# Optimization experiments

Measured on AMD Instinct MI355X. Metric: run time of the kernel, lower is better.

The kernel has to match this reference:

```python
import jax, jax.numpy as jnp
import numpy as np

E, K, MULT = 8, 2, 4          # num_experts, top_k, ffn mult
CF = 1.25                     # capacity_factor


def setup_inputs() -> dict:
    key = jax.random.key(0)
    ks = jax.random.split(key, 8)
    B, T, C = 4, 2048, 1024
    H = C * MULT
    s = 0.02
    return {
        "x": jax.random.normal(ks[0], (B, T, C), jnp.float32),
        "rw": jax.random.normal(ks[1], (E, C), jnp.float32) * s,   # router weight [E,C]
        "rb": jnp.zeros((E,), jnp.float32),                        # router bias
        "w1": jax.random.normal(ks[2], (E, C, H), jnp.float32) * s,
        "b1": jnp.zeros((E, H), jnp.float32),
        "w2": jax.random.normal(ks[3], (E, H, C), jnp.float32) * s,
        "b2": jnp.zeros((E, C), jnp.float32),
    }


def reference(x, rw, rb, w1, b1, w2, b2):
    B, T, C = x.shape
    N = B * T
    cap = int(CF * N / E)                      # static capacity per expert
    xf = x.reshape(N, C)
    logits = xf @ rw.T + rb                    # [N,E]
    probs = jax.nn.softmax(logits, axis=-1)
    topk_probs, topk_idx = jax.lax.top_k(probs, K)      # [N,K]
    topk_probs = topk_probs / topk_probs.sum(-1, keepdims=True)

    # Flatten (token, choice) row-major == torch.where(mask) ordering
    flat_idx = topk_idx.reshape(-1)            # [N*K] expert id per slot
    flat_gate = topk_probs.reshape(-1)         # [N*K]
    onehot = jax.nn.one_hot(flat_idx, E, dtype=jnp.int32)          # [N*K,E]
    pos = (jnp.cumsum(onehot, axis=0) - 1)[jnp.arange(N * K), flat_idx]  # rank within expert
    keep = pos < cap                           # first-come-first-served capacity drop
    tok = jnp.arange(N * K) // K               # owning token of each slot

    # Dispatch into [E, cap] buffers; dropped slots go to a dump slot at the end
    buf = jnp.where(keep, flat_idx * cap + pos, E * cap)
    gate_buf = jnp.zeros(E * cap + 1, x.dtype).at[buf].add(flat_gate)[:E * cap]
    tok_buf = jnp.zeros(E * cap + 1, jnp.int32).at[buf].set(tok)[:E * cap]

    inp = xf[tok_buf].reshape(E, cap, C)       # gathered expert inputs
    h = jax.nn.gelu(jnp.einsum('eic,ech->eih', inp, w1) + b1[:, None, :], approximate=False)
    out = jnp.einsum('eih,ehc->eic', h, w2) + b2[:, None, :]
    out = out * gate_buf.reshape(E, cap, 1)    # empty slots have gate 0 -> zero contribution

    y = jnp.zeros((N, C), x.dtype).at[tok_buf].add(out.reshape(E * cap, C))

    # Aux load-balancing loss
    imp = probs.sum(0)
    imp = imp / imp.sum()
    load = jnp.minimum(onehot.sum(0).astype(x.dtype), cap)   # kept token counts
    load = load / load.sum()
    aux_loss = (imp * load).sum() * (E ** 2)
    return y.reshape(B, T, C), aux_loss
```

## Files before the change

kernel.cpp:

```cpp
#include <hip/hip_runtime.h>
#include <hip/hip_bf16.h>
#include <math.h>

#define NE    8
#define KTOP  2
#define CDIM  1024
#define HDIM  4096
#define NTOK  8192
#define CAPE  1280
#define NSLOT (NTOK * KTOP)

typedef __bf16 bf16x8 __attribute__((ext_vector_type(8)));
typedef __bf16 bf16x4 __attribute__((ext_vector_type(4)));
typedef __bf16 bf16x2 __attribute__((ext_vector_type(2)));
typedef float  f32x4  __attribute__((ext_vector_type(4)));

#define GAS __attribute__((address_space(1)))
#define LAS __attribute__((address_space(3)))

__global__ __launch_bounds__(256) void k_transpose_bf16(
    const float* __restrict__ src, __bf16* __restrict__ dst, int R, int Cc)
{
    __shared__ float tile[32][33];
    const int e  = blockIdx.z;
    const int cb = blockIdx.x * 32;
    const int rb = blockIdx.y * 32;
    const int t  = threadIdx.x;
    const int tx = t & 31, ty = t >> 5;
    const float* s = src + (size_t)e * R * Cc;
    __bf16*      d = dst + (size_t)e * R * Cc;
#pragma unroll
    for (int i = 0; i < 32; i += 8)
        tile[ty + i][tx] = s[(size_t)(rb + ty + i) * Cc + cb + tx];
    __syncthreads();
    const int op  = t & 15;
    const int oc0 = t >> 4;
#pragma unroll
    for (int j = 0; j < 2; ++j) {
        const int oc = oc0 + j * 16;
        bf16x2 v;
        v[0] = (__bf16)tile[op * 2][oc];
        v[1] = (__bf16)tile[op * 2 + 1][oc];
        *(bf16x2*)(d + (size_t)(cb + oc) * R + rb + op * 2) = v;
    }
}

__global__ __launch_bounds__(256) void k_router(
    const float* __restrict__ x, const float* __restrict__ rw,
    const float* __restrict__ rb, float* __restrict__ probs,
    float* __restrict__ gates, int* __restrict__ tidx)
{
    __shared__ float rws[NE * CDIM];
    const int tid = threadIdx.x;
    for (int i = tid; i < NE * CDIM / 4; i += 256)
        ((float4*)rws)[i] = ((const float4*)rw)[i];
    __syncthreads();

    const int wave = tid >> 6, lane = tid & 63;
    const int n = blockIdx.x * 4 + wave;
    const float* xr = x + (size_t)n * CDIM;

    float acc[NE];
#pragma unroll
    for (int e = 0; e < NE; ++e) acc[e] = 0.f;
    for (int j = 0; j < CDIM / 64; ++j) {
        const float xv = xr[j * 64 + lane];
#pragma unroll
        for (int e = 0; e < NE; ++e) acc[e] += xv * rws[e * CDIM + j * 64 + lane];
    }
#pragma unroll
    for (int off = 32; off > 0; off >>= 1) {
#pragma unroll
        for (int e = 0; e < NE; ++e) acc[e] += __shfl_down(acc[e], off);
    }
    if (lane == 0) {
        float mx = -1e30f;
#pragma unroll
        for (int e = 0; e < NE; ++e) { acc[e] += rb[e]; mx = fmaxf(mx, acc[e]); }
        float p[NE], s = 0.f;
#pragma unroll
        for (int e = 0; e < NE; ++e) { p[e] = expf(acc[e] - mx); s += p[e]; }
        const float inv = 1.f / s;
#pragma unroll
        for (int e = 0; e < NE; ++e) { p[e] *= inv; probs[(size_t)n * NE + e] = p[e]; }
        int   i1 = 0;  float v1 = p[0];
        int   i2 = -1; float v2 = -1.f;
#pragma unroll
        for (int e = 1; e < NE; ++e) {
            if (p[e] > v1)      { v2 = v1; i2 = i1; v1 = p[e]; i1 = e; }
            else if (p[e] > v2) { v2 = p[e]; i2 = e; }
        }
        const float gs = 1.f / (v1 + v2);
        gates[n * 2 + 0] = v1 * gs;  gates[n * 2 + 1] = v2 * gs;
        tidx[n * 2 + 0]  = i1;       tidx[n * 2 + 1]  = i2;
    }
}

__global__ __launch_bounds__(256) void k_scan(
    const int* __restrict__ tidx, const float* __restrict__ probs,
    int* __restrict__ slot, int* __restrict__ tok, float* __restrict__ d_aux)
{
    __shared__ int   lcnt[256][NE];
    __shared__ float ps[256][NE];
    const int t = threadIdx.x;

    for (int i = t; i < NE * CAPE; i += 256) tok[i] = 0;

    int c8[NE];
#pragma unroll
    for (int e = 0; e < NE; ++e) c8[e] = 0;
    const int per  = NSLOT / 256;
    const int base = t * per;
    for (int s = 0; s < per; ++s) c8[tidx[base + s]]++;
#pragma unroll
    for (int e = 0; e < NE; ++e) lcnt[t][e] = c8[e];

    float f8[NE];
#pragma unroll
    for (int e = 0; e < NE; ++e) f8[e] = 0.f;
    for (int n = t; n < NTOK; n += 256) {
        const float4 a = *(const float4*)(probs + (size_t)n * NE);
        const float4 b = *(const float4*)(probs + (size_t)n * NE + 4);
        f8[0] += a.x; f8[1] += a.y; f8[2] += a.z; f8[3] += a.w;
        f8[4] += b.x; f8[5] += b.y; f8[6] += b.z; f8[7] += b.w;
    }
#pragma unroll
    for (int e = 0; e < NE; ++e) ps[t][e] = f8[e];

    __syncthreads();

    int pre[NE], tot[NE];
#pragma unroll
    for (int e = 0; e < NE; ++e) { pre[e] = 0; tot[e] = 0; }
    for (int tt = 0; tt < 256; ++tt) {
#pragma unroll
        for (int e = 0; e < NE; ++e) {
            const int v = lcnt[tt][e];
            tot[e] += v;
            if (tt < t) pre[e] += v;
        }
    }
    for (int s = 0; s < per; ++s) {
        const int sg = base + s;
        const int e  = tidx[sg];
        const int p  = pre[e]++;
        if (p < CAPE) { slot[sg] = e * CAPE + p; tok[e * CAPE + p] = sg >> 1; }
        else          { slot[sg] = -1; }
    }
    if (t == 0) {
        float imp[NE], isum = 0.f, ld[NE], lsum = 0.f;
#pragma unroll
        for (int e = 0; e < NE; ++e) {
            float v = 0.f;
            for (int tt = 0; tt < 256; ++tt) v += ps[tt][e];
            imp[e] = v; isum += v;
        }
#pragma unroll
        for (int e = 0; e < NE; ++e) { ld[e] = fminf((float)tot[e], (float)CAPE); lsum += ld[e]; }
        float aux = 0.f;
#pragma unroll
        for (int e = 0; e < NE; ++e) aux += (imp[e] / isum) * (ld[e] / lsum);
        *d_aux = aux * (float)(NE * NE);
    }
}

__global__ __launch_bounds__(256) void k_gather(
    const float* __restrict__ x, const int* __restrict__ tok,
    __bf16* __restrict__ inp)
{
    const int row = blockIdx.x;
    const int t   = threadIdx.x;
    const int tk  = tok[row];
    const float4 v = ((const float4*)(x + (size_t)tk * CDIM))[t];
    bf16x4 o;
    o[0] = (__bf16)v.x; o[1] = (__bf16)v.y; o[2] = (__bf16)v.z; o[3] = (__bf16)v.w;
    *(bf16x4*)(inp + (size_t)row * CDIM + t * 4) = o;
}

#define MFMA_BF16 __builtin_amdgcn_mfma_f32_16x16x32_bf16
#define DSR(dst, addr, IMM) \
    asm volatile("ds_read_b128 %0, %1 offset:" #IMM : "=v"(dst) : "v"(addr))
#define WLG(N)  asm volatile("s_waitcnt lgkmcnt(" #N ")" ::: "memory")
#define WVM0()  asm volatile("s_waitcnt vmcnt(0)" ::: "memory")
#define SB0()   __builtin_amdgcn_sched_barrier(0)

#define MFMA_PHASE(MB, AR)                                                    \
    __builtin_amdgcn_s_setprio(1);                                            \
    _Pragma("unroll")                                                         \
    for (int mm = 0; mm < 2; ++mm) {                                          \
        _Pragma("unroll")                                                     \
        for (int n = 0; n < 4; ++n) {                                         \
            acc[(MB) + mm][n] = MFMA_BF16(bfr[n][0], AR[mm][0], acc[(MB) + mm][n], 0, 0, 0); \
            acc[(MB) + mm][n] = MFMA_BF16(bfr[n][1], AR[mm][1], acc[(MB) + mm][n], 0, 0, 0); \
        }                                                                     \
    }                                                                         \
    __builtin_amdgcn_s_setprio(0);                                            \
    SB0();

template <bool GELU>
__global__ __launch_bounds__(512, 2) void k_gemm8(
    const __bf16* __restrict__ Aall, const __bf16* __restrict__ Ball,
    const float* __restrict__ biasAll, __bf16* __restrict__ Call,
    int Ktot, int Ntot, int NBN, int mtPerE)
{
    __shared__ char lds[131072];

    const int NK  = Ktot >> 6;
    const int cpx = gridDim.x >> 3;
    const int id  = blockIdx.x;
    const int sid = (id & 7) * cpx + (id >> 3);
    const int bm  = sid / NBN, bn = sid % NBN;
    const int e   = bm / mtPerE;

    const size_t row0 = (size_t)bm * 256;
    const int    col0 = bn * 256;

    const int tid = threadIdx.x;
    const int w   = tid >> 6, l = tid & 63;
    const int wr  = w >> 2, wc = w & 3;
    const int lr  = l & 15, hi = l >> 4;

    const int srow = (w << 3) + (l >> 3);
    const int kf   = ((l & 7) ^ (l >> 3)) << 3;
    const __bf16* pA = Aall + (row0 + srow) * (size_t)Ktot + kf;
    const __bf16* pB = Ball + ((size_t)e * Ntot + col0 + srow) * (size_t)Ktot + kf;
    const size_t rstep = (size_t)64 * Ktot;
    const unsigned L0  = (unsigned)(size_t)(LAS char*)lds;
    const unsigned dA0 = L0 + w * 1024;
    const unsigned dB0 = L0 + 32768 + w * 1024;

    auto STAGE_ALL = [&](unsigned bufbit, int kt) {
        const __bf16* ga = pA + (size_t)kt * 64;
        const __bf16* gb = pB + (size_t)kt * 64;
#pragma unroll
        for (int h = 0; h < 4; ++h)
            __builtin_amdgcn_global_load_lds(
                (const GAS void*)(ga + h * rstep),
                (LAS void*)(size_t)(dA0 + bufbit + h * 8192), 16, 0, 0);
#pragma unroll
        for (int h = 0; h < 4; ++h)
            __builtin_amdgcn_global_load_lds(
                (const GAS void*)(gb + h * rstep),
                (LAS void*)(size_t)(dB0 + bufbit + h * 8192), 16, 0, 0);
    };

    const unsigned swz = (l & 7) << 4;
    const unsigned kb0 = ((unsigned)(hi << 4)) ^ swz;
    const unsigned kb1 = ((unsigned)(64 + (hi << 4))) ^ swz;
    const unsigned Abase = L0 + wr * 16384 + lr * 128;
    const unsigned Bbase = L0 + 32768 + (wc >> 1) * 16384 + (wc & 1) * 8192 + lr * 128;

    STAGE_ALL(0, 0);
    WVM0();
    __builtin_amdgcn_s_barrier();
    SB0();

    f32x4 acc[8][4] = {};
    bf16x8 bfr[4][2], aX[2][2], aY[2][2];

    unsigned cb = 0;
    for (int T = 0; T < NK; ++T) {
        const unsigned nb = cb ^ 65536u;
        const unsigned va0 = Abase + cb + kb0, va1 = Abase + cb + kb1;
        const unsigned vb0 = Bbase + cb + kb0, vb1 = Bbase + cb + kb1;

        DSR(bfr[0][0], vb0, 0);    DSR(bfr[0][1], vb1, 0);
        DSR(bfr[1][0], vb0, 2048); DSR(bfr[1][1], vb1, 2048);
        DSR(bfr[2][0], vb0, 4096); DSR(bfr[2][1], vb1, 4096);
        DSR(bfr[3][0], vb0, 6144); DSR(bfr[3][1], vb1, 6144);
        DSR(aX[0][0], va0, 0);     DSR(aX[0][1], va1, 0);
        DSR(aX[1][0], va0, 2048);  DSR(aX[1][1], va1, 2048);

        if (T + 1 < NK) STAGE_ALL(nb, T + 1);

        DSR(aY[0][0], va0, 4096);  DSR(aY[0][1], va1, 4096);
        DSR(aY[1][0], va0, 6144);  DSR(aY[1][1], va1, 6144);

        WLG(4); SB0();
        MFMA_PHASE(0, aX)
        DSR(aX[0][0], va0, 8192);  DSR(aX[0][1], va1, 8192);
        DSR(aX[1][0], va0, 10240); DSR(aX[1][1], va1, 10240);
        WLG(4); SB0();
        MFMA_PHASE(2, aY)
        DSR(aY[0][0], va0, 12288); DSR(aY[0][1], va1, 12288);
        DSR(aY[1][0], va0, 14336); DSR(aY[1][1], va1, 14336);
        WLG(4); SB0();
        MFMA_PHASE(4, aX)
        WLG(0); SB0();
        MFMA_PHASE(6, aY)

        WVM0();
        __builtin_amdgcn_s_barrier();
        SB0();
        cb = nb;
    }

    const size_t crow0 = row0 + (size_t)wr * 128;
    const int    ccol0 = col0 + wc * 64;
#pragma unroll
    for (int n = 0; n < 4; ++n) {
        float bb[4] = {0.f, 0.f, 0.f, 0.f};
        if (GELU) {
            const float4 b4 = *(const float4*)(biasAll + (size_t)e * Ntot
                                               + ccol0 + n * 16 + hi * 4);
            bb[0] = b4.x; bb[1] = b4.y; bb[2] = b4.z; bb[3] = b4.w;
        }
#pragma unroll
        for (int m = 0; m < 8; ++m) {
            const f32x4 v = acc[m][n];
            bf16x4 o;
#pragma unroll
            for (int i = 0; i < 4; ++i) {
                float t = v[i];
                if (GELU) {
                    t += bb[i];
                    const float u  = 0.7978845608028654f * (t + 0.044715f * t * t * t);
                    const float ex = __expf(2.f * u);
                    t = t * (1.f - 1.f / (ex + 1.f));
                }
                o[i] = (__bf16)t;
            }
            *(bf16x4*)(Call + (crow0 + m * 16 + lr) * (size_t)Ntot
                       + ccol0 + n * 16 + hi * 4) = o;
        }
    }
}

__global__ __launch_bounds__(256) void k_combine(
    const __bf16* __restrict__ outb, const int* __restrict__ slot,
    const float* __restrict__ gates, const int* __restrict__ tidx,
    const float* __restrict__ b2, float* __restrict__ y)
{
    const int n = blockIdx.x;
    const int t = threadIdx.x;
    const int c = t * 4;
    float r0 = 0.f, r1 = 0.f, r2 = 0.f, r3 = 0.f;
#pragma unroll
    for (int k = 0; k < KTOP; ++k) {
        const int s = slot[n * 2 + k];
        if (s < 0) continue;
        const float g = gates[n * 2 + k];
        const int   e = tidx[n * 2 + k];
        const bf16x4 v = *(const bf16x4*)(outb + (size_t)s * CDIM + c);
        const float4 bb = *(const float4*)(b2 + (size_t)e * CDIM + c);
        r0 += g * ((float)v[0] + bb.x);
        r1 += g * ((float)v[1] + bb.y);
        r2 += g * ((float)v[2] + bb.z);
        r3 += g * ((float)v[3] + bb.w);
    }
    float4 o = make_float4(r0, r1, r2, r3);
    *(float4*)(y + (size_t)n * CDIM + c) = o;
}

extern "C" void kernel_launch(void* const* d_in, const int* in_sizes, int n_in,
                              void* d_out, int out_size, void* d_ws, size_t ws_size,
                              hipStream_t stream)
{
    const float* x  = (const float*)d_in[0];
    const float* rw = (const float*)d_in[1];
    const float* rb = (const float*)d_in[2];
    const float* w1 = (const float*)d_in[3];
    const float* b1 = (const float*)d_in[4];
    const float* w2 = (const float*)d_in[5];
    const float* b2 = (const float*)d_in[6];
    float* y = (float*)d_out;

    char* ws = (char*)d_ws;
    size_t off = 0;
    auto alloc = [&](size_t bytes) -> void* {
        void* p = ws + off;
        off = (off + bytes + 255) & ~(size_t)255;
        return p;
    };
    __bf16* w1t  = (__bf16*)alloc((size_t)NE * CDIM * HDIM * 2);
    __bf16* w2t  = (__bf16*)alloc((size_t)NE * CDIM * HDIM * 2);
    __bf16* inp  = (__bf16*)alloc((size_t)NE * CAPE * CDIM * 2);
    __bf16* hbuf = (__bf16*)alloc((size_t)NE * CAPE * HDIM * 2);
    __bf16* outb = (__bf16*)alloc((size_t)NE * CAPE * CDIM * 2);
    float*  probs = (float*)alloc((size_t)NTOK * NE * 4);
    float*  gates = (float*)alloc((size_t)NTOK * 2 * 4);
    int*    tidx  = (int*)alloc((size_t)NTOK * 2 * 4);
    int*    slot  = (int*)alloc((size_t)NTOK * 2 * 4);
    int*    tok   = (int*)alloc((size_t)NE * CAPE * 4);

    k_transpose_bf16<<<dim3(HDIM / 32, CDIM / 32, NE), 256, 0, stream>>>(
        w1, w1t, CDIM, HDIM);
    k_transpose_bf16<<<dim3(CDIM / 32, HDIM / 32, NE), 256, 0, stream>>>(
        w2, w2t, HDIM, CDIM);

    k_router<<<NTOK / 4, 256, 0, stream>>>(x, rw, rb, probs, gates, tidx);

    k_scan<<<1, 256, 0, stream>>>(tidx, probs, slot, tok, y + (size_t)NTOK * CDIM);

    k_gather<<<NE * CAPE, 256, 0, stream>>>(x, tok, inp);

    k_gemm8<true><<<dim3((HDIM / 256) * (NE * CAPE / 256)), 512, 0, stream>>>(
        inp, w1t, b1, hbuf, CDIM, HDIM, HDIM / 256, CAPE / 256);
    k_gemm8<false><<<dim3((CDIM / 256) * (NE * CAPE / 256)), 512, 0, stream>>>(
        hbuf, w2t, nullptr, outb, HDIM, CDIM, CDIM / 256, CAPE / 256);

    k_combine<<<NTOK, 256, 0, stream>>>(outb, slot, gates, tidx, b2, y);
}
```

Before: 427.6 us.

## Retile expert GEMMs to 320x128 blocks with barrier-synchronized two-half k-loop

Changes the expert FFN GEMM tile from 256x256 to 320x128, so each expert's 1280-row capacity maps onto exactly 4 row tiles and the wave layout becomes 4x2 with 5x4 accumulators per wave. The k-loop is rebuilt to read full A/B fragments for each half of the 64-wide k-step, with extra workgroup barriers around each MFMA cluster instead of the staggered lgkmcnt-pipelined phases. This lowers LDS use and register pressure and gives more blocks, at the cost of lower arithmetic intensity per tile and more synchronisation with less LDS/MFMA overlap.

```diff
diff --git a/kernel.cpp b/kernel.cpp
--- a/kernel.cpp
+++ b/kernel.cpp
@@ -180,22 +180,19 @@
 #define MFMA_BF16 __builtin_amdgcn_mfma_f32_16x16x32_bf16
 #define DSR(dst, addr, IMM) \
     asm volatile("ds_read_b128 %0, %1 offset:" #IMM : "=v"(dst) : "v"(addr))
-#define WLG(N)  asm volatile("s_waitcnt lgkmcnt(" #N ")" ::: "memory")
+#define WLG0()  asm volatile("s_waitcnt lgkmcnt(0)" ::: "memory")
 #define WVM0()  asm volatile("s_waitcnt vmcnt(0)" ::: "memory")
 #define SB0()   __builtin_amdgcn_sched_barrier(0)
 
-#define MFMA_PHASE(MB, AR)                                                    \
+#define CLUSTER20()                                                           \
     __builtin_amdgcn_s_setprio(1);                                            \
     _Pragma("unroll")                                                         \
-    for (int mm = 0; mm < 2; ++mm) {                                          \
+    for (int m = 0; m < 5; ++m) {                                             \
         _Pragma("unroll")                                                     \
-        for (int n = 0; n < 4; ++n) {                                         \
-            acc[(MB) + mm][n] = MFMA_BF16(bfr[n][0], AR[mm][0], acc[(MB) + mm][n], 0, 0, 0); \
-            acc[(MB) + mm][n] = MFMA_BF16(bfr[n][1], AR[mm][1], acc[(MB) + mm][n], 0, 0, 0); \
-        }                                                                     \
+        for (int n = 0; n < 4; ++n)                                           \
+            acc[m][n] = MFMA_BF16(fb[n], fa[m], acc[m][n], 0, 0, 0);          \
     }                                                                         \
-    __builtin_amdgcn_s_setprio(0);                                            \
-    SB0();
+    __builtin_amdgcn_s_setprio(0);
 
 template <bool GELU>
 __global__ __launch_bounds__(512, 2) void k_gemm8(
@@ -203,7 +200,7 @@
     const float* __restrict__ biasAll, __bf16* __restrict__ Call,
     int Ktot, int Ntot, int NBN, int mtPerE)
 {
-    __shared__ char lds[131072];
+    __shared__ char lds[114688];
 
     const int NK  = Ktot >> 6;
     const int cpx = gridDim.x >> 3;
@@ -212,12 +209,12 @@
     const int bm  = sid / NBN, bn = sid % NBN;
     const int e   = bm / mtPerE;
 
-    const size_t row0 = (size_t)bm * 256;
-    const int    col0 = bn * 256;
+    const size_t row0 = (size_t)bm * 320;
+    const int    col0 = bn * 128;
 
     const int tid = threadIdx.x;
     const int w   = tid >> 6, l = tid & 63;
-    const int wr  = w >> 2, wc = w & 3;
+    const int wr  = w >> 1, wc = w & 1;
     const int lr  = l & 15, hi = l >> 4;
 
     const int srow = (w << 3) + (l >> 3);
@@ -227,93 +224,86 @@
     const size_t rstep = (size_t)64 * Ktot;
     const unsigned L0  = (unsigned)(size_t)(LAS char*)lds;
     const unsigned dA0 = L0 + w * 1024;
-    const unsigned dB0 = L0 + 32768 + w * 1024;
-
-    auto STAGE_ALL = [&](unsigned bufbit, int kt) {
+    const unsigned dB0 = L0 + 81920 + w * 1024;
+
+    auto STAGE_ALL = [&](unsigned abufo, unsigned bbufo, int kt) {
         const __bf16* ga = pA + (size_t)kt * 64;
         const __bf16* gb = pB + (size_t)kt * 64;
 #pragma unroll
-        for (int h = 0; h < 4; ++h)
+        for (int h = 0; h < 5; ++h)
             __builtin_amdgcn_global_load_lds(
                 (const GAS void*)(ga + h * rstep),
-                (LAS void*)(size_t)(dA0 + bufbit + h * 8192), 16, 0, 0);
-#pragma unroll
-        for (int h = 0; h < 4; ++h)
+                (LAS void*)(size_t)(dA0 + abufo + h * 8192), 16, 0, 0);
+#pragma unroll
+        for (int h = 0; h < 2; ++h)
             __builtin_amdgcn_global_load_lds(
                 (const GAS void*)(gb + h * rstep),
-                (LAS void*)(size_t)(dB0 + bufbit + h * 8192), 16, 0, 0);
+                (LAS void*)(size_t)(dB0 + bbufo + h * 8192), 16, 0, 0);
     };
 
     const unsigned swz = (l & 7) << 4;
     const unsigned kb0 = ((unsigned)(hi << 4)) ^ swz;
     const unsigned kb1 = ((unsigned)(64 + (hi << 4))) ^ swz;
-    const unsigned Abase = L0 + wr * 16384 + lr * 128;
-    const unsigned Bbase = L0 + 32768 + (wc >> 1) * 16384 + (wc & 1) * 8192 + lr * 128;
-
-    STAGE_ALL(0, 0);
+    const unsigned AbaseR = L0 + (unsigned)(wr * 80 + lr) * 128;
+    const unsigned BbaseR = L0 + 81920 + (unsigned)(wc * 64 + lr) * 128;
+
+    STAGE_ALL(0, 0, 0);
     WVM0();
     __builtin_amdgcn_s_barrier();
     SB0();
 
-    f32x4 acc[8][4] = {};
-    bf16x8 bfr[4][2], aX[2][2], aY[2][2];
-
-    unsigned cb = 0;
+    f32x4 acc[5][4] = {};
+    bf16x8 fa[5], fb[4];
+
+    unsigned ab = 0, bb = 0;
     for (int T = 0; T < NK; ++T) {
-        const unsigned nb = cb ^ 65536u;
-        const unsigned va0 = Abase + cb + kb0, va1 = Abase + cb + kb1;
-        const unsigned vb0 = Bbase + cb + kb0, vb1 = Bbase + cb + kb1;
-
-        DSR(bfr[0][0], vb0, 0);    DSR(bfr[0][1], vb1, 0);
-        DSR(bfr[1][0], vb0, 2048); DSR(bfr[1][1], vb1, 2048);
-        DSR(bfr[2][0], vb0, 4096); DSR(bfr[2][1], vb1, 4096);
-        DSR(bfr[3][0], vb0, 6144); DSR(bfr[3][1], vb1, 6144);
-        DSR(aX[0][0], va0, 0);     DSR(aX[0][1], va1, 0);
-        DSR(aX[1][0], va0, 2048);  DSR(aX[1][1], va1, 2048);
-
-        if (T + 1 < NK) STAGE_ALL(nb, T + 1);
-
-        DSR(aY[0][0], va0, 4096);  DSR(aY[0][1], va1, 4096);
-        DSR(aY[1][0], va0, 6144);  DSR(aY[1][1], va1, 6144);
-
-        WLG(4); SB0();
-        MFMA_PHASE(0, aX)
-        DSR(aX[0][0], va0, 8192);  DSR(aX[0][1], va1, 8192);
-        DSR(aX[1][0], va0, 10240); DSR(aX[1][1], va1, 10240);
-        WLG(4); SB0();
-        MFMA_PHASE(2, aY)
-        DSR(aY[0][0], va0, 12288); DSR(aY[0][1], va1, 12288);
-        DSR(aY[1][0], va0, 14336); DSR(aY[1][1], va1, 14336);
-        WLG(4); SB0();
-        MFMA_PHASE(4, aX)
-        WLG(0); SB0();
-        MFMA_PHASE(6, aY)
-
+        const unsigned va0 = AbaseR + ab + kb0, va1 = AbaseR + ab + kb1;
+        const unsigned vb0 = BbaseR + bb + kb0, vb1 = BbaseR + bb + kb1;
+
+        DSR(fa[0], va0, 0);    DSR(fa[1], va0, 2048); DSR(fa[2], va0, 4096);
+        DSR(fa[3], va0, 6144); DSR(fa[4], va0, 8192);
+        DSR(fb[0], vb0, 0);    DSR(fb[1], vb0, 2048);
+        DSR(fb[2], vb0, 4096); DSR(fb[3], vb0, 6144);
+        if (T + 1 < NK) STAGE_ALL(ab ^ 40960u, bb ^ 16384u, T + 1);
+        __builtin_amdgcn_s_barrier();
+        WLG0(); SB0();
+        CLUSTER20()
+        __builtin_amdgcn_s_barrier();
+        SB0();
+
+        DSR(fa[0], va1, 0);    DSR(fa[1], va1, 2048); DSR(fa[2], va1, 4096);
+        DSR(fa[3], va1, 6144); DSR(fa[4], va1, 8192);
+        DSR(fb[0], vb1, 0);    DSR(fb[1], vb1, 2048);
+        DSR(fb[2], vb1, 4096); DSR(fb[3], vb1, 6144);
+        __builtin_amdgcn_s_barrier();
+        WLG0(); SB0();
+        CLUSTER20()
         WVM0();
         __builtin_amdgcn_s_barrier();
         SB0();
-        cb = nb;
-    }
-
-    const size_t crow0 = row0 + (size_t)wr * 128;
+
+        ab ^= 40960u; bb ^= 16384u;
+    }
+
+    const size_t crow0 = row0 + (size_t)wr * 80;
     const int    ccol0 = col0 + wc * 64;
 #pragma unroll
     for (int n = 0; n < 4; ++n) {
-        float bb[4] = {0.f, 0.f, 0.f, 0.f};
+        float bbv[4] = {0.f, 0.f, 0.f, 0.f};
         if (GELU) {
             const float4 b4 = *(const float4*)(biasAll + (size_t)e * Ntot
                                                + ccol0 + n * 16 + hi * 4);
-            bb[0] = b4.x; bb[1] = b4.y; bb[2] = b4.z; bb[3] = b4.w;
-        }
-#pragma unroll
-        for (int m = 0; m < 8; ++m) {
+            bbv[0] = b4.x; bbv[1] = b4.y; bbv[2] = b4.z; bbv[3] = b4.w;
+        }
+#pragma unroll
+        for (int m = 0; m < 5; ++m) {
             const f32x4 v = acc[m][n];
             bf16x4 o;
 #pragma unroll
             for (int i = 0; i < 4; ++i) {
                 float t = v[i];
                 if (GELU) {
-                    t += bb[i];
+                    t += bbv[i];
                     const float u  = 0.7978845608028654f * (t + 0.044715f * t * t * t);
                     const float ex = __expf(2.f * u);
                     t = t * (1.f - 1.f / (ex + 1.f));
@@ -394,10 +384,10 @@
 
     k_gather<<<NE * CAPE, 256, 0, stream>>>(x, tok, inp);
 
-    k_gemm8<true><<<dim3((HDIM / 256) * (NE * CAPE / 256)), 512, 0, stream>>>(
-        inp, w1t, b1, hbuf, CDIM, HDIM, HDIM / 256, CAPE / 256);
-    k_gemm8<false><<<dim3((CDIM / 256) * (NE * CAPE / 256)), 512, 0, stream>>>(
-        hbuf, w2t, nullptr, outb, HDIM, CDIM, CDIM / 256, CAPE / 256);
+    k_gemm8<true><<<dim3((NTOK * KTOP * 10 / 16 / 320) * (HDIM / 128)), 512, 0, stream>>>(
+        inp, w1t, b1, hbuf, CDIM, HDIM, HDIM / 128, 4);
+    k_gemm8<false><<<dim3((NTOK * KTOP * 10 / 16 / 320) * (CDIM / 128)), 512, 0, stream>>>(
+        hbuf, w2t, nullptr, outb, HDIM, CDIM, CDIM / 128, 4);
 
     k_combine<<<NTOK, 256, 0, stream>>>(outb, slot, gates, tidx, b2, y);
 }
```

Result: faster. 407.3 us (-4.7%).

## Switch expert GEMM to 4-wave blocks with 128x128 per-wave tiles

Applied to the files above, without the earlier changes.

Replaces the 8-wave 256x256 GEMM with a 4-wave version. Each wave now computes a 128x128 sub-tile with 64 accumulators, which raises the ratio of MFMA work to LDS fragment reads. The LDS read and MFMA interleaving is rebuilt as four quad phases, and the setprio hints are dropped. The cost is heavy register pressure (256 accumulator floats plus 32 fragment registers) at one block per CU, so latency hiding has to come from the software pipeline alone.

```diff
diff --git a/kernel.cpp b/kernel.cpp
--- a/kernel.cpp
+++ b/kernel.cpp
@@ -184,21 +184,23 @@
 #define WVM0()  asm volatile("s_waitcnt vmcnt(0)" ::: "memory")
 #define SB0()   __builtin_amdgcn_sched_barrier(0)
 
-#define MFMA_PHASE(MB, AR)                                                    \
-    __builtin_amdgcn_s_setprio(1);                                            \
+#define QUAD(FA, FB, NB)                                                      \
     _Pragma("unroll")                                                         \
-    for (int mm = 0; mm < 2; ++mm) {                                          \
+    for (int n = 0; n < 4; ++n) {                                             \
         _Pragma("unroll")                                                     \
-        for (int n = 0; n < 4; ++n) {                                         \
-            acc[(MB) + mm][n] = MFMA_BF16(bfr[n][0], AR[mm][0], acc[(MB) + mm][n], 0, 0, 0); \
-            acc[(MB) + mm][n] = MFMA_BF16(bfr[n][1], AR[mm][1], acc[(MB) + mm][n], 0, 0, 0); \
-        }                                                                     \
+        for (int m = 0; m < 8; ++m)                                           \
+            acc[m][(NB) + n] =                                                \
+                MFMA_BF16(FB[(NB) + n], FA[m], acc[m][(NB) + n], 0, 0, 0);    \
     }                                                                         \
-    __builtin_amdgcn_s_setprio(0);                                            \
     SB0();
 
+#define RD_A(FA, VA)                                                          \
+    DSR(FA[0], VA, 0);     DSR(FA[1], VA, 2048);  DSR(FA[2], VA, 4096);       \
+    DSR(FA[3], VA, 6144);  DSR(FA[4], VA, 8192);  DSR(FA[5], VA, 10240);      \
+    DSR(FA[6], VA, 12288); DSR(FA[7], VA, 14336);
+
 template <bool GELU>
-__global__ __launch_bounds__(512, 2) void k_gemm8(
+__global__ __launch_bounds__(256, 1) void k_gemm4(
     const __bf16* __restrict__ Aall, const __bf16* __restrict__ Ball,
     const float* __restrict__ biasAll, __bf16* __restrict__ Call,
     int Ktot, int Ntot, int NBN, int mtPerE)
@@ -217,93 +219,92 @@
 
     const int tid = threadIdx.x;
     const int w   = tid >> 6, l = tid & 63;
-    const int wr  = w >> 2, wc = w & 3;
     const int lr  = l & 15, hi = l >> 4;
 
-    const int srow = (w << 3) + (l >> 3);
-    const int kf   = ((l & 7) ^ (l >> 3)) << 3;
+    const int srow = tid >> 3;
+    const int kf   = ((tid & 7) ^ (srow & 7)) << 3;
     const __bf16* pA = Aall + (row0 + srow) * (size_t)Ktot + kf;
     const __bf16* pB = Ball + ((size_t)e * Ntot + col0 + srow) * (size_t)Ktot + kf;
-    const size_t rstep = (size_t)64 * Ktot;
+    const size_t rstep = (size_t)32 * Ktot;
     const unsigned L0  = (unsigned)(size_t)(LAS char*)lds;
     const unsigned dA0 = L0 + w * 1024;
     const unsigned dB0 = L0 + 32768 + w * 1024;
 
-    auto STAGE_ALL = [&](unsigned bufbit, int kt) {
+    auto STAGE = [&](unsigned bo, int kt) {
         const __bf16* ga = pA + (size_t)kt * 64;
         const __bf16* gb = pB + (size_t)kt * 64;
 #pragma unroll
-        for (int h = 0; h < 4; ++h)
+        for (int h = 0; h < 8; ++h) {
             __builtin_amdgcn_global_load_lds(
                 (const GAS void*)(ga + h * rstep),
-                (LAS void*)(size_t)(dA0 + bufbit + h * 8192), 16, 0, 0);
-#pragma unroll
-        for (int h = 0; h < 4; ++h)
+                (LAS void*)(size_t)(dA0 + bo + h * 4096), 16, 0, 0);
             __builtin_amdgcn_global_load_lds(
                 (const GAS void*)(gb + h * rstep),
-                (LAS void*)(size_t)(dB0 + bufbit + h * 8192), 16, 0, 0);
+                (LAS void*)(size_t)(dB0 + bo + h * 4096), 16, 0, 0);
+        }
     };
 
     const unsigned swz = (l & 7) << 4;
     const unsigned kb0 = ((unsigned)(hi << 4)) ^ swz;
     const unsigned kb1 = ((unsigned)(64 + (hi << 4))) ^ swz;
-    const unsigned Abase = L0 + wr * 16384 + lr * 128;
-    const unsigned Bbase = L0 + 32768 + (wc >> 1) * 16384 + (wc & 1) * 8192 + lr * 128;
-
-    STAGE_ALL(0, 0);
+    const unsigned AbaseR = L0 + (unsigned)(((w >> 1) * 128 + lr) * 128);
+    const unsigned BbaseR = L0 + 32768 + (unsigned)(((w & 1) * 128 + lr) * 128);
+
+    STAGE(0, 0);
     WVM0();
     __builtin_amdgcn_s_barrier();
     SB0();
 
-    f32x4 acc[8][4] = {};
-    bf16x8 bfr[4][2], aX[2][2], aY[2][2];
-
-    unsigned cb = 0;
+    f32x4 acc[8][8] = {};
+    bf16x8 fa0[8], fa1[8], fb0[8], fb1[8];
+
+    unsigned bo = 0;
     for (int T = 0; T < NK; ++T) {
-        const unsigned nb = cb ^ 65536u;
-        const unsigned va0 = Abase + cb + kb0, va1 = Abase + cb + kb1;
-        const unsigned vb0 = Bbase + cb + kb0, vb1 = Bbase + cb + kb1;
-
-        DSR(bfr[0][0], vb0, 0);    DSR(bfr[0][1], vb1, 0);
-        DSR(bfr[1][0], vb0, 2048); DSR(bfr[1][1], vb1, 2048);
-        DSR(bfr[2][0], vb0, 4096); DSR(bfr[2][1], vb1, 4096);
-        DSR(bfr[3][0], vb0, 6144); DSR(bfr[3][1], vb1, 6144);
-        DSR(aX[0][0], va0, 0);     DSR(aX[0][1], va1, 0);
-        DSR(aX[1][0], va0, 2048);  DSR(aX[1][1], va1, 2048);
-
-        if (T + 1 < NK) STAGE_ALL(nb, T + 1);
-
-        DSR(aY[0][0], va0, 4096);  DSR(aY[0][1], va1, 4096);
-        DSR(aY[1][0], va0, 6144);  DSR(aY[1][1], va1, 6144);
-
-        WLG(4); SB0();
-        MFMA_PHASE(0, aX)
-        DSR(aX[0][0], va0, 8192);  DSR(aX[0][1], va1, 8192);
-        DSR(aX[1][0], va0, 10240); DSR(aX[1][1], va1, 10240);
-        WLG(4); SB0();
-        MFMA_PHASE(2, aY)
-        DSR(aY[0][0], va0, 12288); DSR(aY[0][1], va1, 12288);
-        DSR(aY[1][0], va0, 14336); DSR(aY[1][1], va1, 14336);
-        WLG(4); SB0();
-        MFMA_PHASE(4, aX)
-        WLG(0); SB0();
-        MFMA_PHASE(6, aY)
+        const unsigned va0 = AbaseR + bo + kb0, va1 = AbaseR + bo + kb1;
+        const unsigned vb0 = BbaseR + bo + kb0, vb1 = BbaseR + bo + kb1;
+
+        RD_A(fa0, va0)
+        DSR(fb0[0], vb0, 0);    DSR(fb0[1], vb0, 2048);
+        DSR(fb0[2], vb0, 4096); DSR(fb0[3], vb0, 6144);
+        DSR(fb0[4], vb0, 8192);  DSR(fb0[5], vb0, 10240);
+        DSR(fb0[6], vb0, 12288); DSR(fb0[7], vb0, 14336);
+
+        if (T + 1 < NK) STAGE(bo ^ 65536u, T + 1);
+
+        WLG(4);  SB0();
+        QUAD(fa0, fb0, 0)
+
+        RD_A(fa1, va1)
+        DSR(fb1[0], vb1, 0);    DSR(fb1[1], vb1, 2048);
+        DSR(fb1[2], vb1, 4096); DSR(fb1[3], vb1, 6144);
+
+        WLG(12); SB0();
+        QUAD(fa0, fb0, 4)
+
+        DSR(fb1[4], vb1, 8192);  DSR(fb1[5], vb1, 10240);
+        DSR(fb1[6], vb1, 12288); DSR(fb1[7], vb1, 14336);
+
+        WLG(4);  SB0();
+        QUAD(fa1, fb1, 0)
+
+        WLG(0);  SB0();
+        QUAD(fa1, fb1, 4)
 
         WVM0();
         __builtin_amdgcn_s_barrier();
         SB0();
-        cb = nb;
-    }
-
-    const size_t crow0 = row0 + (size_t)wr * 128;
-    const int    ccol0 = col0 + wc * 64;
-#pragma unroll
-    for (int n = 0; n < 4; ++n) {
-        float bb[4] = {0.f, 0.f, 0.f, 0.f};
+        bo ^= 65536u;
+    }
+
+    const size_t crow0 = row0 + (size_t)(w >> 1) * 128;
+    const int    ccol0 = col0 + (w & 1) * 128;
+#pragma unroll
+    for (int n = 0; n < 8; ++n) {
+        float bbv[4] = {0.f, 0.f, 0.f, 0.f};
         if (GELU) {
             const float4 b4 = *(const float4*)(biasAll + (size_t)e * Ntot
                                                + ccol0 + n * 16 + hi * 4);
-            bb[0] = b4.x; bb[1] = b4.y; bb[2] = b4.z; bb[3] = b4.w;
+            bbv[0] = b4.x; bbv[1] = b4.y; bbv[2] = b4.z; bbv[3] = b4.w;
         }
 #pragma unroll
         for (int m = 0; m < 8; ++m) {
@@ -313,7 +314,7 @@
             for (int i = 0; i < 4; ++i) {
                 float t = v[i];
                 if (GELU) {
-                    t += bb[i];
+                    t += bbv[i];
                     const float u  = 0.7978845608028654f * (t + 0.044715f * t * t * t);
                     const float ex = __expf(2.f * u);
                     t = t * (1.f - 1.f / (ex + 1.f));
@@ -394,9 +395,9 @@
 
     k_gather<<<NE * CAPE, 256, 0, stream>>>(x, tok, inp);
 
-    k_gemm8<true><<<dim3((HDIM / 256) * (NE * CAPE / 256)), 512, 0, stream>>>(
+    k_gemm4<true><<<dim3((NE * CAPE / 256) * (HDIM / 256)), 256, 0, stream>>>(
         inp, w1t, b1, hbuf, CDIM, HDIM, HDIM / 256, CAPE / 256);
-    k_gemm8<false><<<dim3((CDIM / 256) * (NE * CAPE / 256)), 512, 0, stream>>>(
+    k_gemm4<false><<<dim3((NE * CAPE / 256) * (CDIM / 256)), 256, 0, stream>>>(
         hbuf, w2t, nullptr, outb, HDIM, CDIM, CDIM / 256, CAPE / 256);
 
     k_combine<<<NTOK, 256, 0, stream>>>(outb, slot, gates, tidx, b2, y);
```

Result: slower. 457.0 us (+6.9%).

## Restructure GEMM mainloop into finer-grained half-tile staged pipeline with per-phase barriers

Applied to the files above, without the earlier changes.

The bf16 expert GEMM mainloop is rewritten so that A and B tiles are staged in 128-row halves across four LDS regions, with each of eight phases per two-k-step iteration issuing one half-tile global-to-LDS prefetch and one MFMA block. The goal is to overlap global loads with compute more continuously instead of staging a whole tile and draining vmcnt(0) once per k-step. The cost is many more workgroup barriers per iteration and more intricate waitcnt bookkeeping. Correctness depends on NK being even and on the clamped t2/t3 indices near the end of the loop.

```diff
diff --git a/kernel.cpp b/kernel.cpp
--- a/kernel.cpp
+++ b/kernel.cpp
@@ -178,24 +178,40 @@
 }
 
 #define MFMA_BF16 __builtin_amdgcn_mfma_f32_16x16x32_bf16
-#define DSR(dst, addr, IMM) \
+#define DSR_I(dst, addr, IMM) \
     asm volatile("ds_read_b128 %0, %1 offset:" #IMM : "=v"(dst) : "v"(addr))
-#define WLG(N)  asm volatile("s_waitcnt lgkmcnt(" #N ")" ::: "memory")
-#define WVM0()  asm volatile("s_waitcnt vmcnt(0)" ::: "memory")
-#define SB0()   __builtin_amdgcn_sched_barrier(0)
-
-#define MFMA_PHASE(MB, AR)                                                    \
-    __builtin_amdgcn_s_setprio(1);                                            \
-    _Pragma("unroll")                                                         \
-    for (int mm = 0; mm < 2; ++mm) {                                          \
+#define DSR(dst, addr, IMM) DSR_I(dst, addr, IMM)
+#define WVM4() asm volatile("s_waitcnt vmcnt(4)" ::: "memory")
+#define SB0()  __builtin_amdgcn_sched_barrier(0)
+
+#define PH(RDB, OA0, OA1, MB, VA0, VA1, VB0, VB1, STG, VMW)                   \
+    {                                                                         \
+        if (RDB) {                                                            \
+            DSR(fb[0][0], VB0, 0);    DSR(fb[0][1], VB1, 0);                  \
+            DSR(fb[1][0], VB0, 2048); DSR(fb[1][1], VB1, 2048);               \
+            DSR(fb[2][0], VB0, 4096); DSR(fb[2][1], VB1, 4096);               \
+            DSR(fb[3][0], VB0, 6144); DSR(fb[3][1], VB1, 6144);               \
+        }                                                                     \
+        DSR(fa[0][0], VA0, OA0); DSR(fa[0][1], VA1, OA0);                     \
+        DSR(fa[1][0], VA0, OA1); DSR(fa[1][1], VA1, OA1);                     \
+        STG;                                                                  \
+        if (RDB) { asm volatile("s_waitcnt lgkmcnt(8)" ::: "memory"); }       \
+        __builtin_amdgcn_s_barrier();                                         \
+        asm volatile("s_waitcnt lgkmcnt(0)" ::: "memory");                    \
+        SB0();                                                                \
+        __builtin_amdgcn_s_setprio(1);                                        \
         _Pragma("unroll")                                                     \
         for (int n = 0; n < 4; ++n) {                                         \
-            acc[(MB) + mm][n] = MFMA_BF16(bfr[n][0], AR[mm][0], acc[(MB) + mm][n], 0, 0, 0); \
-            acc[(MB) + mm][n] = MFMA_BF16(bfr[n][1], AR[mm][1], acc[(MB) + mm][n], 0, 0, 0); \
+            acc[MB][n]   = MFMA_BF16(fb[n][0], fa[0][0], acc[MB][n], 0,0,0);  \
+            acc[MB][n]   = MFMA_BF16(fb[n][1], fa[0][1], acc[MB][n], 0,0,0);  \
+            acc[MB+1][n] = MFMA_BF16(fb[n][0], fa[1][0], acc[MB+1][n],0,0,0); \
+            acc[MB+1][n] = MFMA_BF16(fb[n][1], fa[1][1], acc[MB+1][n],0,0,0); \
         }                                                                     \
-    }                                                                         \
-    __builtin_amdgcn_s_setprio(0);                                            \
-    SB0();
+        __builtin_amdgcn_s_setprio(0);                                        \
+        VMW;                                                                  \
+        __builtin_amdgcn_s_barrier();                                        \
+        SB0();                                                                \
+    }
 
 template <bool GELU>
 __global__ __launch_bounds__(512, 2) void k_gemm8(
@@ -206,6 +222,7 @@
     __shared__ char lds[131072];
 
     const int NK  = Ktot >> 6;
+    const int NI  = NK >> 1;
     const int cpx = gridDim.x >> 3;
     const int id  = blockIdx.x;
     const int sid = (id & 7) * cpx + (id >> 3);
@@ -220,90 +237,82 @@
     const int wr  = w >> 2, wc = w & 3;
     const int lr  = l & 15, hi = l >> 4;
 
-    const int srow = (w << 3) + (l >> 3);
-    const int kf   = ((l & 7) ^ (l >> 3)) << 3;
+    const int srow = tid >> 3;
+    const int kf   = ((tid & 7) ^ (srow & 7)) << 3;
     const __bf16* pA = Aall + (row0 + srow) * (size_t)Ktot + kf;
     const __bf16* pB = Ball + ((size_t)e * Ntot + col0 + srow) * (size_t)Ktot + kf;
-    const size_t rstep = (size_t)64 * Ktot;
-    const unsigned L0  = (unsigned)(size_t)(LAS char*)lds;
-    const unsigned dA0 = L0 + w * 1024;
-    const unsigned dB0 = L0 + 32768 + w * 1024;
-
-    auto STAGE_ALL = [&](unsigned bufbit, int kt) {
-        const __bf16* ga = pA + (size_t)kt * 64;
-        const __bf16* gb = pB + (size_t)kt * 64;
-#pragma unroll
-        for (int h = 0; h < 4; ++h)
+    const unsigned L0 = (unsigned)(size_t)(LAS char*)lds;
+
+    const unsigned sA00 = L0 +          w * 1024;
+    const unsigned sA01 = sA00 + 16384;
+    const unsigned sA10 = sA00 + 32768;
+    const unsigned sA11 = sA00 + 49152;
+    const unsigned sB00 = sA00 + 65536;
+    const unsigned sB01 = sB00 + 16384;
+    const unsigned sB10 = sB00 + 32768;
+    const unsigned sB11 = sB00 + 49152;
+
+    auto SH_A = [&](unsigned dbase, int half, int kt) {
+        const __bf16* g = pA + (size_t)(half * 128) * Ktot + (size_t)kt * 64;
+#pragma unroll
+        for (int gg = 0; gg < 2; ++gg)
             __builtin_amdgcn_global_load_lds(
-                (const GAS void*)(ga + h * rstep),
-                (LAS void*)(size_t)(dA0 + bufbit + h * 8192), 16, 0, 0);
-#pragma unroll
-        for (int h = 0; h < 4; ++h)
+                (const GAS void*)(g + (size_t)gg * 64 * Ktot),
+                (LAS void*)(size_t)(dbase + gg * 8192), 16, 0, 0);
+    };
+    auto SH_B = [&](unsigned dbase, int half, int kt) {
+        const __bf16* g = pB + (size_t)(half * 128) * Ktot + (size_t)kt * 64;
+#pragma unroll
+        for (int gg = 0; gg < 2; ++gg)
             __builtin_amdgcn_global_load_lds(
-                (const GAS void*)(gb + h * rstep),
-                (LAS void*)(size_t)(dB0 + bufbit + h * 8192), 16, 0, 0);
+                (const GAS void*)(g + (size_t)gg * 64 * Ktot),
+                (LAS void*)(size_t)(dbase + gg * 8192), 16, 0, 0);
     };
 
     const unsigned swz = (l & 7) << 4;
     const unsigned kb0 = ((unsigned)(hi << 4)) ^ swz;
     const unsigned kb1 = ((unsigned)(64 + (hi << 4))) ^ swz;
-    const unsigned Abase = L0 + wr * 16384 + lr * 128;
-    const unsigned Bbase = L0 + 32768 + (wc >> 1) * 16384 + (wc & 1) * 8192 + lr * 128;
-
-    STAGE_ALL(0, 0);
-    WVM0();
+    const unsigned vA00 = L0 + (unsigned)(wr * 16384 + lr * 128) + kb0;
+    const unsigned vA01 = L0 + (unsigned)(wr * 16384 + lr * 128) + kb1;
+    const unsigned vA10 = vA00 + 32768, vA11 = vA01 + 32768;
+    const unsigned vBb  = L0 + 65536
+        + (unsigned)((wc >> 1) * 16384 + ((wc & 1) * 64 + lr) * 128);
+    const unsigned vB00 = vBb + kb0, vB01 = vBb + kb1;
+    const unsigned vB10 = vB00 + 32768, vB11 = vB01 + 32768;
+
+    SH_B(sB00, 0, 0); SH_B(sB01, 1, 0);
+    SH_A(sA00, 0, 0); SH_A(sA01, 1, 0);
+    SH_B(sB10, 0, 1); SH_B(sB11, 1, 1);
+    WVM4();
     __builtin_amdgcn_s_barrier();
     SB0();
 
     f32x4 acc[8][4] = {};
-    bf16x8 bfr[4][2], aX[2][2], aY[2][2];
-
-    unsigned cb = 0;
-    for (int T = 0; T < NK; ++T) {
-        const unsigned nb = cb ^ 65536u;
-        const unsigned va0 = Abase + cb + kb0, va1 = Abase + cb + kb1;
-        const unsigned vb0 = Bbase + cb + kb0, vb1 = Bbase + cb + kb1;
-
-        DSR(bfr[0][0], vb0, 0);    DSR(bfr[0][1], vb1, 0);
-        DSR(bfr[1][0], vb0, 2048); DSR(bfr[1][1], vb1, 2048);
-        DSR(bfr[2][0], vb0, 4096); DSR(bfr[2][1], vb1, 4096);
-        DSR(bfr[3][0], vb0, 6144); DSR(bfr[3][1], vb1, 6144);
-        DSR(aX[0][0], va0, 0);     DSR(aX[0][1], va1, 0);
-        DSR(aX[1][0], va0, 2048);  DSR(aX[1][1], va1, 2048);
-
-        if (T + 1 < NK) STAGE_ALL(nb, T + 1);
-
-        DSR(aY[0][0], va0, 4096);  DSR(aY[0][1], va1, 4096);
-        DSR(aY[1][0], va0, 6144);  DSR(aY[1][1], va1, 6144);
-
-        WLG(4); SB0();
-        MFMA_PHASE(0, aX)
-        DSR(aX[0][0], va0, 8192);  DSR(aX[0][1], va1, 8192);
-        DSR(aX[1][0], va0, 10240); DSR(aX[1][1], va1, 10240);
-        WLG(4); SB0();
-        MFMA_PHASE(2, aY)
-        DSR(aY[0][0], va0, 12288); DSR(aY[0][1], va1, 12288);
-        DSR(aY[1][0], va0, 14336); DSR(aY[1][1], va1, 14336);
-        WLG(4); SB0();
-        MFMA_PHASE(4, aX)
-        WLG(0); SB0();
-        MFMA_PHASE(6, aY)
-
-        WVM0();
-        __builtin_amdgcn_s_barrier();
-        SB0();
-        cb = nb;
+    bf16x8 fa[2][2], fb[4][2];
+
+    for (int i = 0; i < NI; ++i) {
+        const int t1 = 2 * i + 1;
+        const int t2 = (2 * i + 2 < NK) ? 2 * i + 2 : NK - 1;
+        const int t3 = (2 * i + 3 < NK) ? 2 * i + 3 : NK - 1;
+        PH(1, 0,     2048,  0, vA00, vA01, vB00, vB01, SH_A(sA10, 0, t1), (void)0)
+        PH(0, 4096,  6144,  2, vA00, vA01, vB00, vB01, SH_A(sA11, 1, t1), (void)0)
+        PH(0, 8192,  10240, 4, vA00, vA01, vB00, vB01, SH_B(sB00, 0, t2), (void)0)
+        PH(0, 12288, 14336, 6, vA00, vA01, vB00, vB01, SH_B(sB01, 1, t2), WVM4())
+        PH(1, 0,     2048,  0, vA10, vA11, vB10, vB11, SH_A(sA00, 0, t2), (void)0)
+        PH(0, 4096,  6144,  2, vA10, vA11, vB10, vB11, SH_A(sA01, 1, t2), (void)0)
+        PH(0, 8192,  10240, 4, vA10, vA11, vB10, vB11, SH_B(sB10, 0, t3), (void)0)
+        PH(0, 12288, 14336, 6, vA10, vA11, vB10, vB11, SH_B(sB11, 1, t3), WVM4())
     }
 
     const size_t crow0 = row0 + (size_t)wr * 128;
     const int    ccol0 = col0 + wc * 64;
 #pragma unroll
     for (int n = 0; n < 4; ++n) {
-        float bb[4] = {0.f, 0.f, 0.f, 0.f};
+        float bbv[4] = {0.f, 0.f, 0.f, 0.f};
         if (GELU) {
             const float4 b4 = *(const float4*)(biasAll + (size_t)e * Ntot
                                                + ccol0 + n * 16 + hi * 4);
-            bb[0] = b4.x; bb[1] = b4.y; bb[2] = b4.z; bb[3] = b4.w;
+            bbv[0] = b4.x; bbv[1] = b4.y; bbv[2] = b4.z; bbv[3] = b4.w;
         }
 #pragma unroll
         for (int m = 0; m < 8; ++m) {
@@ -313,7 +322,7 @@
             for (int i = 0; i < 4; ++i) {
                 float t = v[i];
                 if (GELU) {
-                    t += bb[i];
+                    t += bbv[i];
                     const float u  = 0.7978845608028654f * (t + 0.044715f * t * t * t);
                     const float ex = __expf(2.f * u);
                     t = t * (1.f - 1.f / (ex + 1.f));
@@ -394,9 +403,9 @@
 
     k_gather<<<NE * CAPE, 256, 0, stream>>>(x, tok, inp);
 
-    k_gemm8<true><<<dim3((HDIM / 256) * (NE * CAPE / 256)), 512, 0, stream>>>(
+    k_gemm8<true><<<dim3((NE * CAPE / 256) * (HDIM / 256)), 512, 0, stream>>>(
         inp, w1t, b1, hbuf, CDIM, HDIM, HDIM / 256, CAPE / 256);
-    k_gemm8<false><<<dim3((CDIM / 256) * (NE * CAPE / 256)), 512, 0, stream>>>(
+    k_gemm8<false><<<dim3((NE * CAPE / 256) * (CDIM / 256)), 512, 0, stream>>>(
         hbuf, w2t, nullptr, outb, HDIM, CDIM, CDIM / 256, CAPE / 256);
 
     k_combine<<<NTOK, 256, 0, stream>>>(outb, slot, gates, tidx, b2, y);
```

Measured after the change: 417.3 us. 1.02x faster.
